# Optimization experiments

Hardware: AMD Instinct MI355X
Metric: run time of the kernel (lower is better)

## Reference

```python
import jax, jax.numpy as jnp
import numpy as np

B, C, H, W = 16, 256, 56, 56
G, K, R = 16, 3, 2
CR = C // R          # reduced channels = 128
KKG = K * K * G      # span output channels = 144
EPS = 1e-5


def setup_inputs() -> dict:
    key = jax.random.key(0)
    ks = jax.random.split(key, 5)
    return {
        "x": jax.random.normal(ks[0], (B, C, H, W), jnp.float32),
        "w_reduce": jax.random.normal(ks[1], (CR, C), jnp.float32) * 0.05,
        "b_reduce": jax.random.normal(ks[2], (CR,), jnp.float32) * 0.05,
        "gamma": jnp.ones((CR,), jnp.float32),
        "beta": jnp.zeros((CR,), jnp.float32),
        "w_span": jax.random.normal(ks[3], (KKG, CR), jnp.float32) * 0.05,
        "b_span": jax.random.normal(ks[4], (KKG,), jnp.float32) * 0.05,
    }


def _conv1x1(x, w, bias):
    # 1x1 conv == channel contraction
    return jnp.einsum('bchw,oc->bohw', x, w) + bias[None, :, None, None]


def _involution(x, w_reduce, b_reduce, gamma, beta, w_span, b_span):
    b, c, h, w = x.shape
    # kernel-generation branch: reduce -> BN (batch stats) -> ReLU -> span
    t = _conv1x1(x, w_reduce, b_reduce)
    mu = t.mean(axis=(0, 2, 3), keepdims=True)
    var = t.var(axis=(0, 2, 3), keepdims=True)  # biased, as torch BN training
    t = (t - mu) * jax.lax.rsqrt(var + EPS)
    t = t * gamma[None, :, None, None] + beta[None, :, None, None]
    t = jax.nn.relu(t)
    kern = _conv1x1(t, w_span, b_span)  # [b, k*k*g, h, w]
    # 'b (k j g) h w -> b g (k j) h w'
    kern = kern.reshape(b, K, K, G, h, w).transpose(0, 3, 1, 2, 4, 5)
    kern = kern.reshape(b, G, K * K, h, w)
    # unfold x into [b, g, d, k*k, h, w] via shifted padded slices (no dense im2col buffer write pattern beyond necessity)
    p = K // 2
    xp = jnp.pad(x, ((0, 0), (0, 0), (p, p), (p, p)))
    patches = jnp.stack(
        [xp[:, :, i:i + h, j:j + w] for i in range(K) for j in range(K)],
        axis=2)  # [b, c, k*k, h, w]
    patches = patches.reshape(b, G, c // G, K * K, h, w)
    out = jnp.einsum('bgdxhw,bgxhw->bgdhw', patches, kern)  # weighted window sum
    return out.reshape(b, c, h, w)


def reference(x, w_reduce, b_reduce, gamma, beta, w_span, b_span):
    return _involution(x, w_reduce, b_reduce, gamma, beta, w_span, b_span)
```

## Files before the change

kernel.cpp:

```cpp
#include <hip/hip_runtime.h>
#include <hip/hip_bf16.h>

#define B_   16
#define C_   256
#define HW_  3136
#define W_   56
#define CR_  128
#define KKG_ 144
#define G_   16
#define NPOS (B_*HW_)
#define EPS_ 1e-5f
#define NBLK1 1568
#define NBLK3 784

typedef float f32x4 __attribute__((ext_vector_type(4)));
typedef short s16x8 __attribute__((ext_vector_type(8)));

#define T2_OFF_B    0
#define KERN_OFF_B  12845056
#define GP_OFF_B    27295744
#define STAT_OFF_B  28901376
#define WBFR_OFF_B  28902400
#define WBFS_OFF_B  28967936

__device__ inline unsigned short f2bf(float f) {
    unsigned u = __float_as_uint(f);
    u += 0x7fff + ((u >> 16) & 1);
    return (unsigned short)(u >> 16);
}
__device__ inline float bf2f(unsigned short h) {
    return __uint_as_float(((unsigned)h) << 16);
}
__device__ inline unsigned pkcvt(float a, float b) {
    float2 f2; f2.x = a; f2.y = b;
    __hip_bfloat162 h = __float22bfloat162_rn(f2);
    union { __hip_bfloat162 h2; unsigned u; } cv; cv.h2 = h;
    return cv.u;
}

__global__ __launch_bounds__(256) void prep_cast(
    const float* __restrict__ w_reduce, const float* __restrict__ w_span,
    unsigned short* __restrict__ wbfr, unsigned short* __restrict__ wbfs)
{
    int idx = blockIdx.x * 256 + threadIdx.x;
    if (idx < 32768) {
        wbfr[idx] = f2bf(w_reduce[idx]);
    } else {
        int k = idx - 32768;
        if (k < 18432) wbfs[k] = f2bf(w_span[k]);
    }
}

__global__ __launch_bounds__(256, 5) void reduce_mfma(
    const float* __restrict__ x, const unsigned short* __restrict__ wbfr,
    unsigned short* __restrict__ t2, float* __restrict__ gp)
{
    __shared__ float redp[128][2], redq[128][2];

    const int tid = threadIdx.x;
    const int lane = tid & 63, wv = tid >> 6;
    const int q = lane >> 4, i = lane & 15;
    const int q8 = q * 8;
    const int ow = (wv & 1) * 64;
    const int psel = wv >> 1;
    const int blk = blockIdx.x;
    const int b = blk / 98;
    const int p0 = (blk % 98) * 32;
    const int pw = p0 + psel * 16;

    const float* xcol = x + (size_t)b * C_ * HW_ + pw + i;
    const unsigned short* wrow = wbfr + (size_t)(ow + i) * C_ + q8;

    f32x4 acc[4] = {};

    float Bc[8], Bn[8];
    s16x8 Ac[4], An[4];
    #pragma unroll
    for (int k = 0; k < 8; k++) Bc[k] = xcol[(size_t)(q8 + k) * HW_];
    #pragma unroll
    for (int mt = 0; mt < 4; mt++)
        Ac[mt] = *(const s16x8*)(wrow + (size_t)mt * 16 * C_);

    #pragma unroll
    for (int ch = 0; ch < 8; ch++) {
        const int c0 = ch * 32;
        if (ch < 7) {
            #pragma unroll
            for (int k = 0; k < 8; k++)
                Bn[k] = xcol[(size_t)(c0 + 32 + q8 + k) * HW_];
            #pragma unroll
            for (int mt = 0; mt < 4; mt++)
                An[mt] = *(const s16x8*)(wrow + (size_t)mt * 16 * C_ + c0 + 32);
        }
        union { s16x8 v; unsigned u[4]; } Bv;
        #pragma unroll
        for (int k2 = 0; k2 < 4; k2++) Bv.u[k2] = pkcvt(Bc[2*k2], Bc[2*k2+1]);
        #pragma unroll
        for (int mt = 0; mt < 4; mt++)
            acc[mt] = __builtin_amdgcn_mfma_f32_16x16x32_bf16(
                Ac[mt], Bv.v, acc[mt], 0, 0, 0);
        #pragma unroll
        for (int k = 0; k < 8; k++) Bc[k] = Bn[k];
        #pragma unroll
        for (int mt = 0; mt < 4; mt++) Ac[mt] = An[mt];
    }

    const int p = pw + i;
    #pragma unroll
    for (int mt = 0; mt < 4; mt++) {
        uint2 pr;
        pr.x = pkcvt(acc[mt][0], acc[mt][1]);
        pr.y = pkcvt(acc[mt][2], acc[mt][3]);
        *(uint2*)(t2 + ((size_t)b * HW_ + p) * CR_ + ow + mt * 16 + q * 4) = pr;
        #pragma unroll
        for (int reg = 0; reg < 4; reg++) {
            float v = acc[mt][reg];
            float s = v, ss = v * v;
            #pragma unroll
            for (int m = 1; m < 16; m <<= 1) {
                s  += __shfl_xor(s, m);
                ss += __shfl_xor(ss, m);
            }
            if (i == 0) {
                int o = ow + mt * 16 + q * 4 + reg;
                redp[o][psel] = s;
                redq[o][psel] = ss;
            }
        }
    }
    __syncthreads();
    if (tid < 128)
        gp[(size_t)tid * NBLK1 + blk] = redp[tid][0] + redp[tid][1];
    else
        gp[(size_t)tid * NBLK1 + blk] = redq[tid - 128][0] + redq[tid - 128][1];
}

__global__ __launch_bounds__(256) void bn_finalize(
    const float* __restrict__ gp, const float* __restrict__ gamma,
    const float* __restrict__ beta, float* __restrict__ stats)
{
    const int o = blockIdx.x;
    const int tid = threadIdx.x;
    float s = 0.f, ss = 0.f;
    for (int idx = tid; idx < NBLK1; idx += 256) {
        s  += gp[(size_t)o * NBLK1 + idx];
        ss += gp[(size_t)(128 + o) * NBLK1 + idx];
    }
    #pragma unroll
    for (int m = 1; m < 64; m <<= 1) {
        s  += __shfl_xor(s, m);
        ss += __shfl_xor(ss, m);
    }
    __shared__ float rs[4], rss[4];
    if ((tid & 63) == 0) { rs[tid >> 6] = s; rss[tid >> 6] = ss; }
    __syncthreads();
    if (tid == 0) {
        s  = rs[0] + rs[1] + rs[2] + rs[3];
        ss = rss[0] + rss[1] + rss[2] + rss[3];
        float inv_n = 1.0f / (float)NPOS;
        float mu = s * inv_n;
        float var = ss * inv_n - mu * mu;
        float sc = gamma[o] * rsqrtf(var + EPS_);
        stats[o] = sc;
        stats[128 + o] = beta[o] - mu * sc;
    }
}

__global__ __launch_bounds__(256, 3) void span_mfma(
    const unsigned short* __restrict__ t2, const unsigned short* __restrict__ wbfs,
    const float* __restrict__ b_span, const float* __restrict__ stats,
    unsigned short* __restrict__ kern)
{
    __shared__ float scs[128], shs[128], bsp[144];

    const int tid = threadIdx.x;
    const int lane = tid & 63, wv = tid >> 6;
    const int q = lane >> 4, i = lane & 15;
    const int q8 = q * 8;
    const int blk = blockIdx.x;
    const int b = blk / 49;
    const int pw = (blk % 49) * 64 + wv * 16;

    const unsigned short* trow = t2 + ((size_t)b * HW_ + pw + i) * CR_ + q8;
    const unsigned short* wrow = wbfs + (size_t)i * CR_ + q8;

    s16x8 Bc, Bn;
    s16x8 Ac[9], An[9];
    Bc = *(const s16x8*)trow;
    #pragma unroll
    for (int mt = 0; mt < 9; mt++)
        Ac[mt] = *(const s16x8*)(wrow + (size_t)mt * 16 * CR_);

    if (tid < 128) {
        scs[tid] = stats[tid];
        shs[tid] = stats[128 + tid];
    }
    if (tid < 144) bsp[tid] = b_span[tid];
    __syncthreads();

    f32x4 acc[9] = {};

    #pragma unroll
    for (int ch = 0; ch < 4; ch++) {
        const int c0 = ch * 32;
        if (ch < 3) {
            Bn = *(const s16x8*)(trow + c0 + 32);
            #pragma unroll
            for (int mt = 0; mt < 9; mt++)
                An[mt] = *(const s16x8*)(wrow + (size_t)mt * 16 * CR_ + c0 + 32);
        }
        const int cb = c0 + q8;
        float f[8];
        #pragma unroll
        for (int k = 0; k < 8; k++)
            f[k] = fmaxf(fmaf(bf2f((unsigned short)Bc[k]),
                              scs[cb + k], shs[cb + k]), 0.0f);
        union { s16x8 v; unsigned u[4]; } Bv;
        #pragma unroll
        for (int k2 = 0; k2 < 4; k2++) Bv.u[k2] = pkcvt(f[2*k2], f[2*k2+1]);

        #pragma unroll
        for (int mt = 0; mt < 9; mt++)
            acc[mt] = __builtin_amdgcn_mfma_f32_16x16x32_bf16(
                Ac[mt], Bv.v, acc[mt], 0, 0, 0);
        Bc = Bn;
        #pragma unroll
        for (int mt = 0; mt < 9; mt++) Ac[mt] = An[mt];
    }

    const int p = pw + i;
    #pragma unroll
    for (int mt = 0; mt < 9; mt++) {
        #pragma unroll
        for (int reg = 0; reg < 4; reg++) {
            int o2 = mt * 16 + q * 4 + reg;
            int row = (o2 & 15) * 9 + (o2 >> 4);
            kern[((size_t)b * KKG_ + row) * HW_ + p] = f2bf(acc[mt][reg] + bsp[o2]);
        }
    }
}

__global__ __launch_bounds__(256) void involution_apply(
    const float* __restrict__ x, const unsigned short* __restrict__ kern,
    float* __restrict__ out)
{
    int gtid = blockIdx.x * 256 + threadIdx.x;
    int pix = gtid % HW_;
    int bg  = gtid / HW_;
    int g = bg & 15;
    int b = bg >> 4;
    int h = pix / W_;
    int w = pix % W_;

    const unsigned short* kb = kern + ((size_t)(b * G_ + g) * 9) * HW_ + pix;
    float kv[9];
    #pragma unroll
    for (int kk = 0; kk < 9; kk++)
        kv[kk] = bf2f(kb[(size_t)kk * HW_]);

    float acc[16];
    #pragma unroll
    for (int d = 0; d < 16; d++) acc[d] = 0.0f;

    const float* xb = x + (size_t)(b * C_ + g * 16) * HW_;
    #pragma unroll
    for (int di = 0; di < 3; di++) {
        int hh = h + di - 1;
        if (hh < 0 || hh >= W_) continue;
        #pragma unroll
        for (int dj = 0; dj < 3; dj++) {
            int ww = w + dj - 1;
            if (ww < 0 || ww >= W_) continue;
            float kval = kv[di * 3 + dj];
            int off = hh * W_ + ww;
            #pragma unroll
            for (int d = 0; d < 16; d++)
                acc[d] = fmaf(xb[(size_t)d * HW_ + off], kval, acc[d]);
        }
    }
    float* ob = out + (size_t)(b * C_ + g * 16) * HW_ + pix;
    #pragma unroll
    for (int d = 0; d < 16; d++) ob[(size_t)d * HW_] = acc[d];
}

extern "C" void kernel_launch(void* const* d_in, const int* in_sizes, int n_in,
                              void* d_out, int out_size, void* d_ws, size_t ws_size,
                              hipStream_t stream) {
    const float* x        = (const float*)d_in[0];
    const float* w_reduce = (const float*)d_in[1];
    const float* gamma    = (const float*)d_in[3];
    const float* beta     = (const float*)d_in[4];
    const float* w_span   = (const float*)d_in[5];
    const float* b_span   = (const float*)d_in[6];
    float* out = (float*)d_out;

    char* wsb = (char*)d_ws;
    unsigned short* t2   = (unsigned short*)(wsb + T2_OFF_B);
    unsigned short* kern = (unsigned short*)(wsb + KERN_OFF_B);
    float*          gp    = (float*)(wsb + GP_OFF_B);
    float*          stats = (float*)(wsb + STAT_OFF_B);
    unsigned short* wbfr = (unsigned short*)(wsb + WBFR_OFF_B);
    unsigned short* wbfs = (unsigned short*)(wsb + WBFS_OFF_B);

    prep_cast<<<200, 256, 0, stream>>>(w_reduce, w_span, wbfr, wbfs);
    reduce_mfma<<<NBLK1, 256, 0, stream>>>(x, wbfr, t2, gp);
    bn_finalize<<<128, 256, 0, stream>>>(gp, gamma, beta, stats);
    span_mfma<<<NBLK3, 256, 0, stream>>>(t2, wbfs, b_span, stats, kern);
    involution_apply<<<(B_ * G_ * HW_) / 256, 256, 0, stream>>>(x, kern, out);
}
```

Before: 192.3 us.

## Stage reduce and span GEMM operands through LDS with async global_load_lds triple buffering

Both the reduce and span MFMA kernels now copy their activation and weight tiles into shared memory with global_load_lds. The tiles use XOR-swizzled layouts and a three-deep buffer ring, with explicit vmcnt waits and raw barriers. Before this, each lane loaded its own operands from global memory into registers with strided per-lane reads, which gave poor coalescing, especially for the channel-strided x reads. The change adds LDS usage, lowers reduce occupancy from 5 to 4 blocks per SU, and depends on hand-written waitcnt counts being exactly right.

```diff
diff --git a/kernel.cpp b/kernel.cpp
--- a/kernel.cpp
+++ b/kernel.cpp
@@ -38,6 +38,17 @@
     return cv.u;
 }
 
+typedef const __attribute__((address_space(1))) unsigned int* gas_t;
+typedef __attribute__((address_space(3))) unsigned int* las_t;
+__device__ inline void gload_lds16(const void* g, void* l) {
+    __builtin_amdgcn_global_load_lds((gas_t)g, (las_t)l, 16, 0, 0);
+}
+__device__ inline void barrier_raw() {
+    __builtin_amdgcn_sched_barrier(0);
+    __builtin_amdgcn_s_barrier();
+    __builtin_amdgcn_sched_barrier(0);
+}
+
 __global__ __launch_bounds__(256) void prep_cast(
     const float* __restrict__ w_reduce, const float* __restrict__ w_span,
     unsigned short* __restrict__ wbfr, unsigned short* __restrict__ wbfs)
@@ -51,67 +62,89 @@
     }
 }
 
-__global__ __launch_bounds__(256, 5) void reduce_mfma(
+__global__ __launch_bounds__(256, 4) void reduce_mfma(
     const float* __restrict__ x, const unsigned short* __restrict__ wbfr,
     unsigned short* __restrict__ t2, float* __restrict__ gp)
 {
+    __shared__ __align__(16) float xb3[3][1024];
+    __shared__ __align__(16) short awb[3][4096];
     __shared__ float redp[128][2], redq[128][2];
 
     const int tid = threadIdx.x;
     const int lane = tid & 63, wv = tid >> 6;
     const int q = lane >> 4, i = lane & 15;
     const int q8 = q * 8;
-    const int ow = (wv & 1) * 64;
-    const int psel = wv >> 1;
+    const int mrow = (wv & 1) * 64;
+    const int pw = (wv >> 1) * 16;
     const int blk = blockIdx.x;
     const int b = blk / 98;
     const int p0 = (blk % 98) * 32;
-    const int pw = p0 + psel * 16;
-
-    const float* xcol = x + (size_t)b * C_ * HW_ + pw + i;
-    const unsigned short* wrow = wbfr + (size_t)(ow + i) * C_ + q8;
+
+    const int c_st = tid >> 3;
+    const int swz = ((tid & 7) ^ ((c_st >> 1) & 7)) * 4;
+    const float* xlane = x + (size_t)b * C_ * HW_ + (size_t)c_st * HW_ + p0 + swz;
+    const unsigned short* wA0 = wbfr + (size_t)(tid >> 2) * C_ + (tid & 3) * 8;
+    const unsigned short* wA1 = wA0 + (size_t)64 * C_;
+    float* xdst_base = (float*)0;
+    const int wvu4 = (tid & ~63) * 4;
+    const int wvu8 = (tid & ~63) * 8;
+
+    #define STAGE1(ch, bi) do {                                          \
+        gload_lds16(xlane + (size_t)(ch) * 32 * HW_, &xb3[bi][wvu4]);    \
+        gload_lds16(wA0 + (ch) * 32, &awb[bi][wvu8]);                    \
+        gload_lds16(wA1 + (ch) * 32, &awb[bi][2048 + wvu8]);             \
+    } while (0)
+
+    const int p_loc = pw + i;
+    const int pg = p_loc >> 2, pe = p_loc & 3;
 
     f32x4 acc[4] = {};
 
-    float Bc[8], Bn[8];
-    s16x8 Ac[4], An[4];
-    #pragma unroll
-    for (int k = 0; k < 8; k++) Bc[k] = xcol[(size_t)(q8 + k) * HW_];
-    #pragma unroll
-    for (int mt = 0; mt < 4; mt++)
-        Ac[mt] = *(const s16x8*)(wrow + (size_t)mt * 16 * C_);
+    STAGE1(0, 0);
+    STAGE1(1, 1);
 
     #pragma unroll
     for (int ch = 0; ch < 8; ch++) {
-        const int c0 = ch * 32;
-        if (ch < 7) {
-            #pragma unroll
-            for (int k = 0; k < 8; k++)
-                Bn[k] = xcol[(size_t)(c0 + 32 + q8 + k) * HW_];
-            #pragma unroll
-            for (int mt = 0; mt < 4; mt++)
-                An[mt] = *(const s16x8*)(wrow + (size_t)mt * 16 * C_ + c0 + 32);
+        const int cur = ch % 3;
+        if (ch < 7) asm volatile("s_waitcnt vmcnt(3)" ::: "memory");
+        else        asm volatile("s_waitcnt vmcnt(0)" ::: "memory");
+        barrier_raw();
+        if (ch == 0) STAGE1(2, 2);
+        if (ch == 1) STAGE1(3, 0);
+        if (ch == 2) STAGE1(4, 1);
+        if (ch == 3) STAGE1(5, 2);
+        if (ch == 4) STAGE1(6, 0);
+        if (ch == 5) STAGE1(7, 1);
+
+        s16x8 af[4];
+        #pragma unroll
+        for (int mt = 0; mt < 4; mt++)
+            af[mt] = *(const s16x8*)&awb[cur][(mrow + mt * 16 + i) * 32 + q8];
+        float f[8];
+        #pragma unroll
+        for (int k = 0; k < 8; k++) {
+            int cl = q8 + k;
+            int slot = pg ^ ((cl >> 1) & 7);
+            f[k] = xb3[cur][cl * 32 + slot * 4 + pe];
         }
         union { s16x8 v; unsigned u[4]; } Bv;
         #pragma unroll
-        for (int k2 = 0; k2 < 4; k2++) Bv.u[k2] = pkcvt(Bc[2*k2], Bc[2*k2+1]);
+        for (int k2 = 0; k2 < 4; k2++) Bv.u[k2] = pkcvt(f[2*k2], f[2*k2+1]);
+
         #pragma unroll
         for (int mt = 0; mt < 4; mt++)
             acc[mt] = __builtin_amdgcn_mfma_f32_16x16x32_bf16(
-                Ac[mt], Bv.v, acc[mt], 0, 0, 0);
-        #pragma unroll
-        for (int k = 0; k < 8; k++) Bc[k] = Bn[k];
-        #pragma unroll
-        for (int mt = 0; mt < 4; mt++) Ac[mt] = An[mt];
-    }
-
-    const int p = pw + i;
+                af[mt], Bv.v, acc[mt], 0, 0, 0);
+    }
+    #undef STAGE1
+
+    const int p = p0 + pw + i;
     #pragma unroll
     for (int mt = 0; mt < 4; mt++) {
         uint2 pr;
         pr.x = pkcvt(acc[mt][0], acc[mt][1]);
         pr.y = pkcvt(acc[mt][2], acc[mt][3]);
-        *(uint2*)(t2 + ((size_t)b * HW_ + p) * CR_ + ow + mt * 16 + q * 4) = pr;
+        *(uint2*)(t2 + ((size_t)b * HW_ + p) * CR_ + mrow + mt * 16 + q * 4) = pr;
         #pragma unroll
         for (int reg = 0; reg < 4; reg++) {
             float v = acc[mt][reg];
@@ -122,9 +155,9 @@
                 ss += __shfl_xor(ss, m);
             }
             if (i == 0) {
-                int o = ow + mt * 16 + q * 4 + reg;
-                redp[o][psel] = s;
-                redq[o][psel] = ss;
+                int o = mrow + mt * 16 + q * 4 + reg;
+                redp[o][wv >> 1] = s;
+                redq[o][wv >> 1] = ss;
             }
         }
     }
@@ -171,6 +204,8 @@
     const float* __restrict__ b_span, const float* __restrict__ stats,
     unsigned short* __restrict__ kern)
 {
+    __shared__ __align__(16) short aw[144 * 128];
+    __shared__ __align__(16) short bb3[3][2048];
     __shared__ float scs[128], shs[128], bsp[144];
 
     const int tid = threadIdx.x;
@@ -179,56 +214,59 @@
     const int q8 = q * 8;
     const int blk = blockIdx.x;
     const int b = blk / 49;
-    const int pw = (blk % 49) * 64 + wv * 16;
-
-    const unsigned short* trow = t2 + ((size_t)b * HW_ + pw + i) * CR_ + q8;
-    const unsigned short* wrow = wbfs + (size_t)i * CR_ + q8;
-
-    s16x8 Bc, Bn;
-    s16x8 Ac[9], An[9];
-    Bc = *(const s16x8*)trow;
-    #pragma unroll
-    for (int mt = 0; mt < 9; mt++)
-        Ac[mt] = *(const s16x8*)(wrow + (size_t)mt * 16 * CR_);
-
-    if (tid < 128) {
-        scs[tid] = stats[tid];
-        shs[tid] = stats[128 + tid];
-    }
+    const int p0 = (blk % 49) * 64;
+
+    if (tid < 128) { scs[tid] = stats[tid]; shs[tid] = stats[128 + tid]; }
     if (tid < 144) bsp[tid] = b_span[tid];
     __syncthreads();
 
+    const unsigned short* tlane =
+        t2 + ((size_t)b * HW_ + p0 + (tid >> 2)) * CR_ + (tid & 3) * 8;
+    const int wvu8 = (tid & ~63) * 8;
+
+    #pragma unroll
+    for (int e = 0; e < 9; e++) {
+        int U = tid + e * 256;
+        int r = U >> 4, u = U & 15;
+        gload_lds16(wbfs + (size_t)r * CR_ + ((u ^ (r & 7)) * 8),
+                    &aw[((tid & ~63) + e * 256) * 8]);
+    }
+    gload_lds16(tlane,      &bb3[0][wvu8]);
+    gload_lds16(tlane + 32, &bb3[1][wvu8]);
+
     f32x4 acc[9] = {};
 
     #pragma unroll
     for (int ch = 0; ch < 4; ch++) {
-        const int c0 = ch * 32;
-        if (ch < 3) {
-            Bn = *(const s16x8*)(trow + c0 + 32);
-            #pragma unroll
-            for (int mt = 0; mt < 9; mt++)
-                An[mt] = *(const s16x8*)(wrow + (size_t)mt * 16 * CR_ + c0 + 32);
-        }
-        const int cb = c0 + q8;
+        const int cur = ch % 3;
+        if (ch < 3) asm volatile("s_waitcnt vmcnt(1)" ::: "memory");
+        else        asm volatile("s_waitcnt vmcnt(0)" ::: "memory");
+        barrier_raw();
+        if (ch == 0) gload_lds16(tlane + 64, &bb3[2][wvu8]);
+        if (ch == 1) gload_lds16(tlane + 96, &bb3[0][wvu8]);
+
+        s16x8 raw = *(const s16x8*)&bb3[cur][(wv * 16 + i) * 32 + q8];
+        const int cb = ch * 32 + q8;
         float f[8];
         #pragma unroll
         for (int k = 0; k < 8; k++)
-            f[k] = fmaxf(fmaf(bf2f((unsigned short)Bc[k]),
+            f[k] = fmaxf(fmaf(bf2f((unsigned short)raw[k]),
                               scs[cb + k], shs[cb + k]), 0.0f);
         union { s16x8 v; unsigned u[4]; } Bv;
         #pragma unroll
         for (int k2 = 0; k2 < 4; k2++) Bv.u[k2] = pkcvt(f[2*k2], f[2*k2+1]);
 
         #pragma unroll
-        for (int mt = 0; mt < 9; mt++)
+        for (int mt = 0; mt < 9; mt++) {
+            int r = mt * 16 + i;
+            int slot = (ch * 4 + q) ^ (r & 7);
+            s16x8 af = *(const s16x8*)&aw[r * 128 + slot * 8];
             acc[mt] = __builtin_amdgcn_mfma_f32_16x16x32_bf16(
-                Ac[mt], Bv.v, acc[mt], 0, 0, 0);
-        Bc = Bn;
-        #pragma unroll
-        for (int mt = 0; mt < 9; mt++) Ac[mt] = An[mt];
-    }
-
-    const int p = pw + i;
+                af, Bv.v, acc[mt], 0, 0, 0);
+        }
+    }
+
+    const int p = p0 + wv * 16 + i;
     #pragma unroll
     for (int mt = 0; mt < 9; mt++) {
         #pragma unroll
```

Result: faster. 170.7 us (-11.2%).
